# Performance work log

Measured on AMD Instinct MI355X. Metric: run time of the kernel, lower is better.

The kernel has to match this reference:

```python
import jax, jax.numpy as jnp
import numpy as np

EMBED = 64
HEADS = 8
DHEAD = EMBED // HEADS  # 8
LAYERS = 4
VOCAB = 32000
SEQ = 1024
BATCH = 8
EPS = 1e-5


def setup_inputs() -> dict:
    key = jax.random.key(0)
    ks = jax.random.split(key, 24)
    s = 0.02
    inp = {
        "x": jax.random.randint(ks[0], (BATCH, SEQ), 0, VOCAB),
        "targets": jax.random.randint(ks[1], (BATCH, SEQ), 0, VOCAB),
        "tok_emb": jax.random.normal(ks[2], (VOCAB, EMBED)) * s,
        "pos_emb": jax.random.normal(ks[3], (SEQ, EMBED)) * s,
        # per-layer, per-head q/k/v projections (stored as (in,out) so y = x @ W + b)
        "Wq": jax.random.normal(ks[4], (LAYERS, HEADS, EMBED, DHEAD)) * s,
        "bq": jax.random.normal(ks[5], (LAYERS, HEADS, DHEAD)) * s,
        "Wk": jax.random.normal(ks[6], (LAYERS, HEADS, EMBED, DHEAD)) * s,
        "bk": jax.random.normal(ks[7], (LAYERS, HEADS, DHEAD)) * s,
        "Wv": jax.random.normal(ks[8], (LAYERS, HEADS, EMBED, DHEAD)) * s,
        "bv": jax.random.normal(ks[9], (LAYERS, HEADS, DHEAD)) * s,
        "ln1_g": jnp.ones((LAYERS, EMBED)) + jax.random.normal(ks[10], (LAYERS, EMBED)) * s,
        "ln1_b": jax.random.normal(ks[11], (LAYERS, EMBED)) * s,
        "ln2_g": jnp.ones((LAYERS, EMBED)) + jax.random.normal(ks[12], (LAYERS, EMBED)) * s,
        "ln2_b": jax.random.normal(ks[13], (LAYERS, EMBED)) * s,
        "W1": jax.random.normal(ks[14], (LAYERS, EMBED, 4 * EMBED)) * s,
        "b1": jax.random.normal(ks[15], (LAYERS, 4 * EMBED)) * s,
        "W2": jax.random.normal(ks[16], (LAYERS, 4 * EMBED, EMBED)) * s,
        "b2": jax.random.normal(ks[17], (LAYERS, EMBED)) * s,
        "Wout": jax.random.normal(ks[18], (EMBED, VOCAB)) * s,
        "bout": jax.random.normal(ks[19], (VOCAB,)) * s,
    }
    return inp


def _layernorm(x, g, b):
    mu = jnp.mean(x, axis=-1, keepdims=True)
    var = jnp.var(x, axis=-1, keepdims=True)
    return (x - mu) / jnp.sqrt(var + EPS) * g + b


def _mha(h, Wq, bq, Wk, bk, Wv, bv):
    B, T, C = h.shape
    q = jnp.einsum('btc,hcd->bhtd', h, Wq) + bq[:, None, :]
    k = jnp.einsum('btc,hcd->bhtd', h, Wk) + bk[:, None, :]
    v = jnp.einsum('btc,hcd->bhtd', h, Wv) + bv[:, None, :]
    # FAITHFUL to source: key output is .view(B, C, T) -- a raw reshape, not transpose
    kr = k.reshape(B, HEADS, DHEAD, T)
    w = jnp.einsum('bhtd,bhds->bhts', q, kr)  # [B,H,T,T]
    w = jnp.tril(w)
    w = jnp.where(w == 0, -jnp.inf, w)
    w = jax.nn.softmax(w / np.sqrt(DHEAD), axis=-1)
    o = jnp.einsum('bhts,bhsd->bhtd', w, v)
    return o.transpose(0, 2, 1, 3).reshape(B, T, HEADS * DHEAD)


def _forward(x, targets, tok_emb, pos_emb, Wq, bq, Wk, bk, Wv, bv,
             ln1_g, ln1_b, ln2_g, ln2_b, W1, b1, W2, b2, Wout, bout):
    B, T = x.shape
    h = tok_emb[x] + pos_emb[:T]
    for l in range(LAYERS):
        h = h + _layernorm(_mha(h, Wq[l], bq[l], Wk[l], bk[l], Wv[l], bv[l]), ln1_g[l], ln1_b[l])
        z = _layernorm(h, ln2_g[l], ln2_b[l])
        h = h + jax.nn.relu(z @ W1[l] + b1[l]) @ W2[l] + b2[l]
    logits = h @ Wout + bout  # [B,T,V]
    lp = jax.nn.log_softmax(logits.reshape(B * T, -1), axis=-1)
    nll = -jnp.take_along_axis(lp, targets.reshape(B * T, 1), axis=1)
    loss = jnp.mean(nll)
    return logits, loss


def reference(x, targets, tok_emb, pos_emb, Wq, bq, Wk, bk, Wv, bv,
              ln1_g, ln1_b, ln2_g, ln2_b, W1, b1, W2, b2, Wout, bout):
    return _forward(x, targets, tok_emb, pos_emb, Wq, bq, Wk, bk, Wv, bv,
                    ln1_g, ln1_b, ln2_g, ln2_b, W1, b1, W2, b2, Wout, bout)
```

## Files before the change

### kernel.cpp

```cpp
#include <hip/hip_runtime.h>
#include <hip/hip_bf16.h>
#include <math.h>

#define BB 8
#define TT 1024
#define CC 64
#define HH 8
#define DH 8
#define NLAY 4
#define VV 32000
#define FF 256
#define NR (BB*TT)
#define NLOGIT 262144000
#define NCB 125

typedef unsigned short u16;
typedef unsigned int u32;
typedef __attribute__((ext_vector_type(8))) short short8v;
typedef __attribute__((ext_vector_type(4))) float f32x4;

__device__ __forceinline__ float b2f(u16 u){
  union { float f; u32 i; } c; c.i = ((u32)u) << 16; return c.f;
}
__device__ __forceinline__ u16 f2b(float f){
  union { float f; u32 i; } c; c.f = f;
  u32 x = c.i;
  return (u16)((x + 0x7FFF + ((x >> 16) & 1)) >> 16);
}
__device__ __forceinline__ u32 pack2(float lo, float hi){
  return (u32)f2b(lo) | ((u32)f2b(hi) << 16);
}

__global__ void k_probe(const void* ln1g, int* flag){
  if (threadIdx.x == 0 && blockIdx.x == 0){
    const u16* p = (const u16*)ln1g;
    int cnt = 0;
    for (int i = 0; i < 256; i++){ if ((p[i] >> 8) == 0x3F) cnt++; }
    *flag = (cnt > 192) ? 1 : 0;
  }
}

struct ConvArgs {
  const void* src[18];
  float* dst[18];
  int n[18];
  int blkoff[19];
  const int* flag;
  u16* wt16;
};
__global__ void k_convert(ConvArgs a){
  int isb = *a.flag;
  int bid = blockIdx.x;
  int t = 0;
  while (bid >= a.blkoff[t + 1]) t++;
  int base = (bid - a.blkoff[t]) * 1024 + threadIdx.x;
  const u16* s16 = (const u16*)a.src[t];
  const float* s32 = (const float*)a.src[t];
  float* d = a.dst[t];
  int n = a.n[t];
  #pragma unroll
  for (int e = 0; e < 4; e++){
    int i = base + e * 256;
    if (i < n){
      float v = isb ? b2f(s16[i]) : s32[i];
      d[i] = v;
      if (t == 16){
        int k = i / VV, col = i - k * VV;
        a.wt16[(size_t)col * 64 + k] = f2b(v);
      }
    }
  }
}

__global__ void k_embed(const int* __restrict__ x, const float* __restrict__ tok,
                        const float* __restrict__ pos, float* __restrict__ h){
  int i = blockIdx.x * 256 + threadIdx.x;
  int r = i >> 6, c = i & 63;
  int t = r & (TT - 1);
  h[i] = tok[x[r] * 64 + c] + pos[t * 64 + c];
}

__global__ void k_qkv(const float* __restrict__ h,
                      const float* __restrict__ wq, const float* __restrict__ bq,
                      const float* __restrict__ wk, const float* __restrict__ bk,
                      const float* __restrict__ wv, const float* __restrict__ bv,
                      u16* __restrict__ q16, u16* __restrict__ kp16, u16* __restrict__ vt16){
  __shared__ float hs[4][64];
  int tid = threadIdx.x;
  int row0 = blockIdx.x * 4;
  hs[tid >> 6][tid & 63] = h[row0 * 64 + tid];
  __syncthreads();
  int rr = tid >> 6, o = tid & 63;
  int head = o >> 3, d = o & 7;
  int row = row0 + rr;
  int b = row >> 10, t = row & (TT - 1);
  float aq = bq[head * 8 + d], ak = bk[head * 8 + d], av = bv[head * 8 + d];
  #pragma unroll
  for (int c = 0; c < 64; c++){
    float hv = hs[rr][c];
    aq += hv * wq[(head * 64 + c) * 8 + d];
    ak += hv * wk[(head * 64 + c) * 8 + d];
    av += hv * wv[(head * 64 + c) * 8 + d];
  }
  int bh = b * HH + head;
  q16[((size_t)bh * TT + t) * 8 + d] = f2b(aq * 0.35355339059327378f);
  int i = t * 8 + d;
  kp16[((size_t)bh * TT + (i & 1023)) * 8 + (i >> 10)] = f2b(ak);
  vt16[((size_t)bh * 8 + d) * TT + t] = f2b(av);
}

__global__ void __launch_bounds__(64) k_attn(const u16* __restrict__ q16, const u16* __restrict__ kp16,
                                             const u16* __restrict__ vt16, float* __restrict__ att){
  int lane = threadIdx.x & 63;
  int lr = lane & 15, lg = lane >> 4;
  int bh = blockIdx.y;
  int tb = blockIdx.x * 16;
  int t_g = tb + lr;

  short8v qf = {0,0,0,0,0,0,0,0};
  if (lg == 0) qf = *(const short8v*)(q16 + ((size_t)bh * TT + tb + lr) * 8);

  float m = -1e30f, l = 0.f;
  f32x4 o = {0.f, 0.f, 0.f, 0.f};
  int nchunk = (tb >> 5) + 1;

  for (int c = 0; c < nchunk; c++){
    int s0 = c * 32;
    bool skipB = (s0 + 16 > tb + 15);
    short8v kA = {0,0,0,0,0,0,0,0}, kB = {0,0,0,0,0,0,0,0};
    if (lg == 0){
      kA = *(const short8v*)(kp16 + ((size_t)bh * TT + s0 + lr) * 8);
      if (!skipB) kB = *(const short8v*)(kp16 + ((size_t)bh * TT + s0 + 16 + lr) * 8);
    }
    f32x4 sA = __builtin_amdgcn_mfma_f32_16x16x32_bf16(kA, qf, (f32x4){0.f,0.f,0.f,0.f}, 0, 0, 0);
    f32x4 sB;
    if (!skipB)
      sB = __builtin_amdgcn_mfma_f32_16x16x32_bf16(kB, qf, (f32x4){0.f,0.f,0.f,0.f}, 0, 0, 0);
    else
      sB = (f32x4){-1e30f, -1e30f, -1e30f, -1e30f};

    if (s0 + 15 > tb){
      #pragma unroll
      for (int r = 0; r < 4; r++) if (s0 + lg * 4 + r > t_g) sA[r] = -1e30f;
    }
    if (!skipB && s0 + 31 > tb){
      #pragma unroll
      for (int r = 0; r < 4; r++) if (s0 + 16 + lg * 4 + r > t_g) sB[r] = -1e30f;
    }

    float tm = fmaxf(fmaxf(fmaxf(sA[0], sA[1]), fmaxf(sA[2], sA[3])),
                     fmaxf(fmaxf(sB[0], sB[1]), fmaxf(sB[2], sB[3])));
    tm = fmaxf(tm, __shfl_xor(tm, 16, 64));
    tm = fmaxf(tm, __shfl_xor(tm, 32, 64));
    float mn = fmaxf(m, tm);
    float fac = __expf(m - mn);
    l *= fac;
    {
      float f0 = __shfl(fac, lg * 4 + 0, 64);
      float f1 = __shfl(fac, lg * 4 + 1, 64);
      float f2 = __shfl(fac, lg * 4 + 2, 64);
      float f3 = __shfl(fac, lg * 4 + 3, 64);
      o[0] *= f0; o[1] *= f1; o[2] *= f2; o[3] *= f3;
    }
    f32x4 pA, pB;
    #pragma unroll
    for (int r = 0; r < 4; r++){ pA[r] = __expf(sA[r] - mn); pB[r] = __expf(sB[r] - mn); }
    float ls = pA[0] + pA[1] + pA[2] + pA[3] + pB[0] + pB[1] + pB[2] + pB[3];
    ls += __shfl_xor(ls, 16, 64);
    ls += __shfl_xor(ls, 32, 64);
    l += ls;
    m = mn;

    u32 a0 = pack2(pA[0], pA[1]), a1 = pack2(pA[2], pA[3]);
    u32 b0 = pack2(pB[0], pB[1]), b1 = pack2(pB[2], pB[3]);
    int src0 = ((2 * lg) & 3) * 16 + lr;
    int src1 = src0 + 16;
    u32 A0 = __shfl((int)a0, src0, 64), A1 = __shfl((int)a1, src0, 64);
    u32 A2 = __shfl((int)a0, src1, 64), A3 = __shfl((int)a1, src1, 64);
    u32 B0 = __shfl((int)b0, src0, 64), B1 = __shfl((int)b1, src0, 64);
    u32 B2 = __shfl((int)b0, src1, 64), B3 = __shfl((int)b1, src1, 64);
    union { u32 u[4]; short8v v; } pu;
    if (lg < 2){ pu.u[0] = A0; pu.u[1] = A1; pu.u[2] = A2; pu.u[3] = A3; }
    else       { pu.u[0] = B0; pu.u[1] = B1; pu.u[2] = B2; pu.u[3] = B3; }

    short8v vf = {0,0,0,0,0,0,0,0};
    if (lr < 8) vf = *(const short8v*)(vt16 + ((size_t)bh * 8 + lr) * TT + s0 + lg * 8);

    o = __builtin_amdgcn_mfma_f32_16x16x32_bf16(pu.v, vf, o, 0, 0, 0);
  }

  float linv = 1.f / l;
  float i0 = __shfl(linv, lg * 4 + 0, 64);
  float i1 = __shfl(linv, lg * 4 + 1, 64);
  float i2 = __shfl(linv, lg * 4 + 2, 64);
  float i3 = __shfl(linv, lg * 4 + 3, 64);
  if (lr < 8){
    int b = bh >> 3, head = bh & 7;
    float* op = att + ((size_t)b * TT + tb) * 64 + head * 8 + lr;
    op[(lg * 4 + 0) * 64] = o[0] * i0;
    op[(lg * 4 + 1) * 64] = o[1] * i1;
    op[(lg * 4 + 2) * 64] = o[2] * i2;
    op[(lg * 4 + 3) * 64] = o[3] * i3;
  }
}

__global__ void k_lnres(const float* __restrict__ src, const float* __restrict__ g,
                        const float* __restrict__ bb, float* __restrict__ h){
  int tid = threadIdx.x;
  int row = blockIdx.x * 4 + (tid >> 6);
  int lane = tid & 63;
  float x = src[row * 64 + lane];
  float s = x, sq = x * x;
  for (int msk = 32; msk; msk >>= 1){
    s += __shfl_xor(s, msk, 64);
    sq += __shfl_xor(sq, msk, 64);
  }
  float mu = s * (1.f / 64);
  float var = sq * (1.f / 64) - mu * mu;
  float rstd = rsqrtf(fmaxf(var, 0.f) + 1e-5f);
  h[row * 64 + lane] += (x - mu) * rstd * g[lane] + bb[lane];
}

__global__ void k_ffn(float* __restrict__ h, const float* __restrict__ g, const float* __restrict__ bb,
                      const float* __restrict__ w1, const float* __restrict__ b1,
                      const float* __restrict__ w2, const float* __restrict__ b2){
  __shared__ float z[8][64];
  __shared__ float a[8][256];
  int tid = threadIdx.x;
  int row0 = blockIdx.x * 8;
  {
    int rr = tid >> 5, cp = tid & 31;
    int c0 = cp * 2;
    const float* hp = h + (row0 + rr) * 64;
    float x0 = hp[c0], x1 = hp[c0 + 1];
    float s = x0 + x1, sq = x0 * x0 + x1 * x1;
    for (int msk = 16; msk; msk >>= 1){
      s += __shfl_xor(s, msk, 64);
      sq += __shfl_xor(sq, msk, 64);
    }
    float mu = s * (1.f / 64);
    float var = sq * (1.f / 64) - mu * mu;
    float rstd = rsqrtf(fmaxf(var, 0.f) + 1e-5f);
    z[rr][c0]     = (x0 - mu) * rstd * g[c0] + bb[c0];
    z[rr][c0 + 1] = (x1 - mu) * rstd * g[c0 + 1] + bb[c0 + 1];
  }
  __syncthreads();
  {
    int j = tid;
    float acc[8];
    float bj = b1[j];
    #pragma unroll
    for (int r = 0; r < 8; r++) acc[r] = bj;
    for (int c = 0; c < 64; c++){
      float w = w1[c * 256 + j];
      #pragma unroll
      for (int r = 0; r < 8; r++) acc[r] += z[r][c] * w;
    }
    #pragma unroll
    for (int r = 0; r < 8; r++) a[r][j] = fmaxf(acc[r], 0.f);
  }
  __syncthreads();
  #pragma unroll
  for (int half = 0; half < 2; half++){
    int oi = tid + half * 256;
    int r = oi >> 6, c = oi & 63;
    float acc = b2[c];
    for (int k = 0; k < 256; k++) acc += a[r][k] * w2[k * 64 + c];
    h[(row0 + r) * 64 + c] += acc;
  }
}

__global__ void k_h2b(const float* __restrict__ h, u16* __restrict__ hb){
  int i = blockIdx.x * 256 + threadIdx.x;
  hb[i] = f2b(h[i]);
}

__global__ void __launch_bounds__(256) k_logits(const u16* __restrict__ hb, const u16* __restrict__ wt,
                                                const float* __restrict__ bout, float* __restrict__ logits,
                                                float2* __restrict__ part){
  int tid = threadIdx.x;
  int wave = tid >> 6, lane = tid & 63;
  int lr = lane & 15, lg = lane >> 4;
  int row0 = blockIdx.y * 64;
  int colw = blockIdx.x * 256 + wave * 64;

  short8v af[4][2];
  #pragma unroll
  for (int mi = 0; mi < 4; mi++)
    #pragma unroll
    for (int kk = 0; kk < 2; kk++)
      af[mi][kk] = *(const short8v*)(hb + (row0 + mi * 16 + lr) * 64 + kk * 32 + lg * 8);

  short8v bf[4][2];
  #pragma unroll
  for (int nf = 0; nf < 4; nf++){
    int col = colw + nf * 16 + lr;
    #pragma unroll
    for (int kk = 0; kk < 2; kk++)
      bf[nf][kk] = *(const short8v*)(wt + (size_t)col * 64 + kk * 32 + lg * 8);
  }

  f32x4 acc[4][4];
  #pragma unroll
  for (int mi = 0; mi < 4; mi++)
    #pragma unroll
    for (int nf = 0; nf < 4; nf++)
      acc[mi][nf] = (f32x4){0.f, 0.f, 0.f, 0.f};

  #pragma unroll
  for (int mi = 0; mi < 4; mi++){
    #pragma unroll
    for (int nf = 0; nf < 4; nf++){
      acc[mi][nf] = __builtin_amdgcn_mfma_f32_16x16x32_bf16(af[mi][0], bf[nf][0], acc[mi][nf], 0, 0, 0);
      acc[mi][nf] = __builtin_amdgcn_mfma_f32_16x16x32_bf16(af[mi][1], bf[nf][1], acc[mi][nf], 0, 0, 0);
    }
  }

  float bo[4];
  #pragma unroll
  for (int nf = 0; nf < 4; nf++) bo[nf] = bout[colw + nf * 16 + lr];

  #pragma unroll
  for (int mi = 0; mi < 4; mi++){
    #pragma unroll
    for (int nf = 0; nf < 4; nf++){
      int colg = colw + nf * 16 + lr;
      #pragma unroll
      for (int r = 0; r < 4; r++){
        int rowg = row0 + mi * 16 + lg * 4 + r;
        logits[(size_t)rowg * VV + colg] = acc[mi][nf][r] + bo[nf];
      }
    }
  }

  __shared__ float2 wml[4][64];
  #pragma unroll
  for (int mi = 0; mi < 4; mi++){
    #pragma unroll
    for (int r = 0; r < 4; r++){
      float v0 = acc[mi][0][r] + bo[0], v1 = acc[mi][1][r] + bo[1];
      float v2 = acc[mi][2][r] + bo[2], v3 = acc[mi][3][r] + bo[3];
      float mx = fmaxf(fmaxf(v0, v1), fmaxf(v2, v3));
      for (int msk = 1; msk < 16; msk <<= 1) mx = fmaxf(mx, __shfl_xor(mx, msk, 64));
      float sume = __expf(v0 - mx) + __expf(v1 - mx) + __expf(v2 - mx) + __expf(v3 - mx);
      for (int msk = 1; msk < 16; msk <<= 1) sume += __shfl_xor(sume, msk, 64);
      if (lr == 0) wml[wave][mi * 16 + lg * 4 + r] = make_float2(mx, sume);
    }
  }
  __syncthreads();
  if (tid < 64){
    float M = -1e30f;
    #pragma unroll
    for (int w = 0; w < 4; w++) M = fmaxf(M, wml[w][tid].x);
    float L = 0.f;
    #pragma unroll
    for (int w = 0; w < 4; w++){
      float2 p = wml[w][tid];
      L += p.y * __expf(p.x - M);
    }
    part[(size_t)blockIdx.x * NR + row0 + tid] = make_float2(M, L);
  }
}

__global__ void k_loss(const float2* __restrict__ part, const float* __restrict__ logits,
                       const int* __restrict__ tgt, float* __restrict__ lpart){
  int row = blockIdx.x * 256 + threadIdx.x;
  float M = -1e30f;
  for (int j = 0; j < NCB; j++) M = fmaxf(M, part[(size_t)j * NR + row].x);
  float L = 0.f;
  for (int j = 0; j < NCB; j++){
    float2 p = part[(size_t)j * NR + row];
    L += p.y * __expf(p.x - M);
  }
  float lse = M + __logf(L);
  float tl = logits[(size_t)row * VV + tgt[row]];
  float nll = lse - tl;
  __shared__ float red[4];
  for (int msk = 32; msk; msk >>= 1) nll += __shfl_xor(nll, msk, 64);
  if ((threadIdx.x & 63) == 0) red[threadIdx.x >> 6] = nll;
  __syncthreads();
  if (threadIdx.x == 0) lpart[blockIdx.x] = red[0] + red[1] + red[2] + red[3];
}
__global__ void k_loss2(const float* __restrict__ lpart, float* __restrict__ out){
  if (threadIdx.x == 0 && blockIdx.x == 0){
    float s = 0.f;
    for (int i = 0; i < 32; i++) s += lpart[i];
    out[NLOGIT] = s * (1.f / NR);
  }
}

extern "C" void kernel_launch(void* const* d_in, const int* in_sizes, int n_in,
                              void* d_out, int out_size, void* d_ws, size_t ws_size,
                              hipStream_t stream){
  (void)in_sizes; (void)n_in; (void)out_size; (void)ws_size;
  const int* x = (const int*)d_in[0];
  const int* targets = (const int*)d_in[1];
  float* out = (float*)d_out;

  static const int WN[18] = {2048000, 65536, 16384, 256, 16384, 256, 16384, 256,
                             256, 256, 256, 256, 65536, 1024, 65536, 256, 2048000, 32000};
  char* ws = (char*)d_ws;
  size_t off = 0;
  auto alloc = [&](size_t bytes) -> void* {
    void* p = ws + off;
    off += (bytes + 255) & ~(size_t)255;
    return p;
  };
  int* flag = (int*)alloc(256);
  float* wf[18];
  for (int i = 0; i < 18; i++) wf[i] = (float*)alloc((size_t)WN[i] * 4);
  float* h     = (float*)alloc((size_t)NR * 64 * 4);
  float* att_o = (float*)alloc((size_t)NR * 64 * 4);
  u16* q16     = (u16*)alloc((size_t)NR * 64 * 2);
  u16* kp16    = (u16*)alloc((size_t)NR * 64 * 2);
  u16* vt16    = (u16*)alloc((size_t)NR * 64 * 2);
  u16* hb      = (u16*)alloc((size_t)NR * 64 * 2);
  u16* wt16    = (u16*)alloc((size_t)2048000 * 2);
  float2* part = (float2*)alloc((size_t)NCB * NR * 8);
  float* lpart = (float*)alloc(32 * 4);

  hipLaunchKernelGGL(k_probe, dim3(1), dim3(64), 0, stream, d_in[10], flag);
  ConvArgs ca;
  int blk = 0;
  for (int i = 0; i < 18; i++){
    ca.src[i] = d_in[2 + i];
    ca.dst[i] = wf[i];
    ca.n[i] = WN[i];
    ca.blkoff[i] = blk;
    blk += (WN[i] + 1023) / 1024;
  }
  ca.blkoff[18] = blk;
  ca.flag = flag;
  ca.wt16 = wt16;
  hipLaunchKernelGGL(k_convert, dim3(blk), dim3(256), 0, stream, ca);

  hipLaunchKernelGGL(k_embed, dim3(2048), dim3(256), 0, stream, x, wf[0], wf[1], h);

  for (int l = 0; l < NLAY; l++){
    hipLaunchKernelGGL(k_qkv, dim3(2048), dim3(256), 0, stream, h,
                       wf[2] + l * 4096, wf[3] + l * 64,
                       wf[4] + l * 4096, wf[5] + l * 64,
                       wf[6] + l * 4096, wf[7] + l * 64,
                       q16, kp16, vt16);
    hipLaunchKernelGGL(k_attn, dim3(64, 64), dim3(64), 0, stream, q16, kp16, vt16, att_o);
    hipLaunchKernelGGL(k_lnres, dim3(2048), dim3(256), 0, stream, att_o,
                       wf[8] + l * 64, wf[9] + l * 64, h);
    hipLaunchKernelGGL(k_ffn, dim3(1024), dim3(256), 0, stream, h,
                       wf[10] + l * 64, wf[11] + l * 64,
                       wf[12] + l * 16384, wf[13] + l * 256,
                       wf[14] + l * 16384, wf[15] + l * 64);
  }

  hipLaunchKernelGGL(k_h2b, dim3(2048), dim3(256), 0, stream, h, hb);
  hipLaunchKernelGGL(k_logits, dim3(NCB, 128), dim3(256), 0, stream, hb, wt16, wf[17], out, part);
  hipLaunchKernelGGL(k_loss, dim3(32), dim3(256), 0, stream, part, out, targets, lpart);
  hipLaunchKernelGGL(k_loss2, dim3(1), dim3(64), 0, stream, lpart, out);
}
```

Before: 792.0 us.

## Fuse attention with layernorm-residual, transpose Wout via LDS, restructure logits stores

Several independent changes land together. The probe kernel is folded into a per-block ballot. The scattered Wout transpose inside the convert kernel becomes a separate LDS-tiled transpose kernel. Attention now runs all 8 heads of a batch in one 512-thread block and applies the LN+residual in place, which drops the att_o buffer and the k_lnres launch. The final FFN layer writes the bf16 hidden state directly instead of running k_h2b. The logits MFMA operands are swapped so each lane holds 4 contiguous columns, allowing vectorized nontemporal stores with a new grid order, and the loss reduction launches are reshaped. These changes add code complexity and raise register and LDS pressure in the fused attention block.

Result: faster. 735.2 us (-7.2%).

```diff
diff --git a/kernel.cpp b/kernel.cpp
--- a/kernel.cpp
+++ b/kernel.cpp
@@ -30,14 +30,10 @@
 __device__ __forceinline__ u32 pack2(float lo, float hi){
   return (u32)f2b(lo) | ((u32)f2b(hi) << 16);
 }
-
-__global__ void k_probe(const void* ln1g, int* flag){
-  if (threadIdx.x == 0 && blockIdx.x == 0){
-    const u16* p = (const u16*)ln1g;
-    int cnt = 0;
-    for (int i = 0; i < 256; i++){ if ((p[i] >> 8) == 0x3F) cnt++; }
-    *flag = (cnt > 192) ? 1 : 0;
-  }
+__device__ __forceinline__ int probe_bf16(const void* ln1g){
+  const u16* lp = (const u16*)ln1g;
+  unsigned long long m = __ballot((lp[threadIdx.x & 63] >> 8) == 0x3F);
+  return (__popcll(m) > 48) ? 1 : 0;
 }
 
 struct ConvArgs {
@@ -45,11 +41,9 @@
   float* dst[18];
   int n[18];
   int blkoff[19];
-  const int* flag;
-  u16* wt16;
 };
-__global__ void k_convert(ConvArgs a){
-  int isb = *a.flag;
+__global__ void k_convert(ConvArgs a, const void* ln1g){
+  int isb = probe_bf16(ln1g);
   int bid = blockIdx.x;
   int t = 0;
   while (bid >= a.blkoff[t + 1]) t++;
@@ -61,14 +55,31 @@
   #pragma unroll
   for (int e = 0; e < 4; e++){
     int i = base + e * 256;
-    if (i < n){
-      float v = isb ? b2f(s16[i]) : s32[i];
-      d[i] = v;
-      if (t == 16){
-        int k = i / VV, col = i - k * VV;
-        a.wt16[(size_t)col * 64 + k] = f2b(v);
-      }
-    }
+    if (i < n) d[i] = isb ? b2f(s16[i]) : s32[i];
+  }
+}
+
+__global__ void __launch_bounds__(256) k_trans(const void* __restrict__ wsrc, const void* __restrict__ ln1g,
+                                               u16* __restrict__ wt){
+  __shared__ float ws_[64][65];
+  int tid = threadIdx.x;
+  int isb = probe_bf16(ln1g);
+  int v0 = blockIdx.x * 64;
+  const u16* s16 = (const u16*)wsrc;
+  const float* s32 = (const float*)wsrc;
+  int vl = tid & 63;
+  #pragma unroll
+  for (int kk = 0; kk < 16; kk++){
+    int k = kk * 4 + (tid >> 6);
+    size_t idx = (size_t)k * VV + v0 + vl;
+    ws_[vl][k] = isb ? b2f(s16[idx]) : s32[idx];
+  }
+  __syncthreads();
+  #pragma unroll
+  for (int pass = 0; pass < 16; pass++){
+    int v2 = pass * 4 + (tid >> 6);
+    int k = tid & 63;
+    wt[(size_t)(v0 + v2) * 64 + k] = f2b(ws_[v2][k]);
   }
 }
 
@@ -109,11 +120,16 @@
   vt16[((size_t)bh * 8 + d) * TT + t] = f2b(av);
 }
 
-__global__ void __launch_bounds__(64) k_attn(const u16* __restrict__ q16, const u16* __restrict__ kp16,
-                                             const u16* __restrict__ vt16, float* __restrict__ att){
-  int lane = threadIdx.x & 63;
+__global__ void __launch_bounds__(512) k_attn2(const u16* __restrict__ q16, const u16* __restrict__ kp16,
+                                               const u16* __restrict__ vt16, const float* __restrict__ g,
+                                               const float* __restrict__ be, float* __restrict__ h){
+  __shared__ float ot[16][64];
+  int tid = threadIdx.x;
+  int w = tid >> 6;
+  int lane = tid & 63;
   int lr = lane & 15, lg = lane >> 4;
-  int bh = blockIdx.y;
+  int b = blockIdx.y;
+  int bh = b * HH + w;
   int tb = blockIdx.x * 16;
   int t_g = tb + lr;
 
@@ -195,35 +211,33 @@
   float i2 = __shfl(linv, lg * 4 + 2, 64);
   float i3 = __shfl(linv, lg * 4 + 3, 64);
   if (lr < 8){
-    int b = bh >> 3, head = bh & 7;
-    float* op = att + ((size_t)b * TT + tb) * 64 + head * 8 + lr;
-    op[(lg * 4 + 0) * 64] = o[0] * i0;
-    op[(lg * 4 + 1) * 64] = o[1] * i1;
-    op[(lg * 4 + 2) * 64] = o[2] * i2;
-    op[(lg * 4 + 3) * 64] = o[3] * i3;
-  }
-}
-
-__global__ void k_lnres(const float* __restrict__ src, const float* __restrict__ g,
-                        const float* __restrict__ bb, float* __restrict__ h){
-  int tid = threadIdx.x;
-  int row = blockIdx.x * 4 + (tid >> 6);
-  int lane = tid & 63;
-  float x = src[row * 64 + lane];
-  float s = x, sq = x * x;
-  for (int msk = 32; msk; msk >>= 1){
-    s += __shfl_xor(s, msk, 64);
-    sq += __shfl_xor(sq, msk, 64);
-  }
-  float mu = s * (1.f / 64);
-  float var = sq * (1.f / 64) - mu * mu;
-  float rstd = rsqrtf(fmaxf(var, 0.f) + 1e-5f);
-  h[row * 64 + lane] += (x - mu) * rstd * g[lane] + bb[lane];
+    ot[lg * 4 + 0][w * 8 + lr] = o[0] * i0;
+    ot[lg * 4 + 1][w * 8 + lr] = o[1] * i1;
+    ot[lg * 4 + 2][w * 8 + lr] = o[2] * i2;
+    ot[lg * 4 + 3][w * 8 + lr] = o[3] * i3;
+  }
+  __syncthreads();
+
+  #pragma unroll
+  for (int pass = 0; pass < 2; pass++){
+    int rl = (tid >> 6) + pass * 8;
+    float x = ot[rl][lane];
+    float s = x, sq = x * x;
+    for (int msk = 32; msk; msk >>= 1){
+      s += __shfl_xor(s, msk, 64);
+      sq += __shfl_xor(sq, msk, 64);
+    }
+    float mu = s * (1.f / 64);
+    float var = sq * (1.f / 64) - mu * mu;
+    float rstd = rsqrtf(fmaxf(var, 0.f) + 1e-5f);
+    h[((size_t)b * TT + tb + rl) * 64 + lane] += (x - mu) * rstd * g[lane] + be[lane];
+  }
 }
 
 __global__ void k_ffn(float* __restrict__ h, const float* __restrict__ g, const float* __restrict__ bb,
                       const float* __restrict__ w1, const float* __restrict__ b1,
-                      const float* __restrict__ w2, const float* __restrict__ b2){
+                      const float* __restrict__ w2, const float* __restrict__ b2,
+                      u16* __restrict__ hbo, int last){
   __shared__ float z[8][64];
   __shared__ float a[8][256];
   int tid = threadIdx.x;
@@ -266,13 +280,11 @@
     int r = oi >> 6, c = oi & 63;
     float acc = b2[c];
     for (int k = 0; k < 256; k++) acc += a[r][k] * w2[k * 64 + c];
-    h[(row0 + r) * 64 + c] += acc;
-  }
-}
-
-__global__ void k_h2b(const float* __restrict__ h, u16* __restrict__ hb){
-  int i = blockIdx.x * 256 + threadIdx.x;
-  hb[i] = f2b(h[i]);
+    int gi = (row0 + r) * 64 + c;
+    float nh = h[gi] + acc;
+    h[gi] = nh;
+    if (last) hbo[gi] = f2b(nh);
+  }
 }
 
 __global__ void __launch_bounds__(256) k_logits(const u16* __restrict__ hb, const u16* __restrict__ wt,
@@ -281,71 +293,70 @@
   int tid = threadIdx.x;
   int wave = tid >> 6, lane = tid & 63;
   int lr = lane & 15, lg = lane >> 4;
-  int row0 = blockIdx.y * 64;
-  int colw = blockIdx.x * 256 + wave * 64;
-
-  short8v af[4][2];
-  #pragma unroll
-  for (int mi = 0; mi < 4; mi++)
+  int row0 = blockIdx.x * 64;
+  int cb = blockIdx.y;
+  int colw = cb * 256 + wave * 64;
+
+  short8v hf[4][2];
+  #pragma unroll
+  for (int ri = 0; ri < 4; ri++)
     #pragma unroll
     for (int kk = 0; kk < 2; kk++)
-      af[mi][kk] = *(const short8v*)(hb + (row0 + mi * 16 + lr) * 64 + kk * 32 + lg * 8);
-
-  short8v bf[4][2];
-  #pragma unroll
-  for (int nf = 0; nf < 4; nf++){
-    int col = colw + nf * 16 + lr;
+      hf[ri][kk] = *(const short8v*)(hb + (row0 + ri * 16 + lr) * 64 + kk * 32 + lg * 8);
+
+  short8v wfr[4][2];
+  #pragma unroll
+  for (int vi = 0; vi < 4; vi++)
     #pragma unroll
     for (int kk = 0; kk < 2; kk++)
-      bf[nf][kk] = *(const short8v*)(wt + (size_t)col * 64 + kk * 32 + lg * 8);
-  }
+      wfr[vi][kk] = *(const short8v*)(wt + (size_t)(colw + vi * 16 + lr) * 64 + kk * 32 + lg * 8);
 
   f32x4 acc[4][4];
   #pragma unroll
-  for (int mi = 0; mi < 4; mi++)
-    #pragma unroll
-    for (int nf = 0; nf < 4; nf++)
-      acc[mi][nf] = (f32x4){0.f, 0.f, 0.f, 0.f};
-
-  #pragma unroll
-  for (int mi = 0; mi < 4; mi++){
-    #pragma unroll
-    for (int nf = 0; nf < 4; nf++){
-      acc[mi][nf] = __builtin_amdgcn_mfma_f32_16x16x32_bf16(af[mi][0], bf[nf][0], acc[mi][nf], 0, 0, 0);
-      acc[mi][nf] = __builtin_amdgcn_mfma_f32_16x16x32_bf16(af[mi][1], bf[nf][1], acc[mi][nf], 0, 0, 0);
-    }
-  }
-
-  float bo[4];
-  #pragma unroll
-  for (int nf = 0; nf < 4; nf++) bo[nf] = bout[colw + nf * 16 + lr];
-
-  #pragma unroll
-  for (int mi = 0; mi < 4; mi++){
-    #pragma unroll
-    for (int nf = 0; nf < 4; nf++){
-      int colg = colw + nf * 16 + lr;
+  for (int ri = 0; ri < 4; ri++)
+    #pragma unroll
+    for (int vi = 0; vi < 4; vi++)
+      acc[ri][vi] = (f32x4){0.f, 0.f, 0.f, 0.f};
+
+  #pragma unroll
+  for (int ri = 0; ri < 4; ri++){
+    #pragma unroll
+    for (int vi = 0; vi < 4; vi++){
+      acc[ri][vi] = __builtin_amdgcn_mfma_f32_16x16x32_bf16(wfr[vi][0], hf[ri][0], acc[ri][vi], 0, 0, 0);
+      acc[ri][vi] = __builtin_amdgcn_mfma_f32_16x16x32_bf16(wfr[vi][1], hf[ri][1], acc[ri][vi], 0, 0, 0);
+    }
+  }
+
+  f32x4 bo[4];
+  #pragma unroll
+  for (int vi = 0; vi < 4; vi++)
+    bo[vi] = *(const f32x4*)(bout + colw + vi * 16 + lg * 4);
+
+  __shared__ float2 wml[4][64];
+  #pragma unroll
+  for (int ri = 0; ri < 4; ri++){
+    f32x4 vals[4];
+    #pragma unroll
+    for (int vi = 0; vi < 4; vi++){
+      vals[vi] = acc[ri][vi] + bo[vi];
+      __builtin_nontemporal_store(vals[vi],
+        (f32x4*)(logits + (size_t)(row0 + ri * 16 + lr) * VV + colw + vi * 16 + lg * 4));
+    }
+    float mx = -1e30f;
+    #pragma unroll
+    for (int vi = 0; vi < 4; vi++)
       #pragma unroll
-      for (int r = 0; r < 4; r++){
-        int rowg = row0 + mi * 16 + lg * 4 + r;
-        logits[(size_t)rowg * VV + colg] = acc[mi][nf][r] + bo[nf];
-      }
-    }
-  }
-
-  __shared__ float2 wml[4][64];
-  #pragma unroll
-  for (int mi = 0; mi < 4; mi++){
-    #pragma unroll
-    for (int r = 0; r < 4; r++){
-      float v0 = acc[mi][0][r] + bo[0], v1 = acc[mi][1][r] + bo[1];
-      float v2 = acc[mi][2][r] + bo[2], v3 = acc[mi][3][r] + bo[3];
-      float mx = fmaxf(fmaxf(v0, v1), fmaxf(v2, v3));
-      for (int msk = 1; msk < 16; msk <<= 1) mx = fmaxf(mx, __shfl_xor(mx, msk, 64));
-      float sume = __expf(v0 - mx) + __expf(v1 - mx) + __expf(v2 - mx) + __expf(v3 - mx);
-      for (int msk = 1; msk < 16; msk <<= 1) sume += __shfl_xor(sume, msk, 64);
-      if (lr == 0) wml[wave][mi * 16 + lg * 4 + r] = make_float2(mx, sume);
-    }
+      for (int r = 0; r < 4; r++) mx = fmaxf(mx, vals[vi][r]);
+    mx = fmaxf(mx, __shfl_xor(mx, 16, 64));
+    mx = fmaxf(mx, __shfl_xor(mx, 32, 64));
+    float sume = 0.f;
+    #pragma unroll
+    for (int vi = 0; vi < 4; vi++)
+      #pragma unroll
+      for (int r = 0; r < 4; r++) sume += __expf(vals[vi][r] - mx);
+    sume += __shfl_xor(sume, 16, 64);
+    sume += __shfl_xor(sume, 32, 64);
+    if (lg == 0) wml[wave][ri * 16 + lr] = make_float2(mx, sume);
   }
   __syncthreads();
   if (tid < 64){
@@ -358,13 +369,13 @@
       float2 p = wml[w][tid];
       L += p.y * __expf(p.x - M);
     }
-    part[(size_t)blockIdx.x * NR + row0 + tid] = make_float2(M, L);
+    part[(size_t)cb * NR + row0 + tid] = make_float2(M, L);
   }
 }
 
 __global__ void k_loss(const float2* __restrict__ part, const float* __restrict__ logits,
                        const int* __restrict__ tgt, float* __restrict__ lpart){
-  int row = blockIdx.x * 256 + threadIdx.x;
+  int row = blockIdx.x * 64 + (threadIdx.x & 63);
   float M = -1e30f;
   for (int j = 0; j < NCB; j++) M = fmaxf(M, part[(size_t)j * NR + row].x);
   float L = 0.f;
@@ -375,18 +386,14 @@
   float lse = M + __logf(L);
   float tl = logits[(size_t)row * VV + tgt[row]];
   float nll = lse - tl;
-  __shared__ float red[4];
   for (int msk = 32; msk; msk >>= 1) nll += __shfl_xor(nll, msk, 64);
-  if ((threadIdx.x & 63) == 0) red[threadIdx.x >> 6] = nll;
-  __syncthreads();
-  if (threadIdx.x == 0) lpart[blockIdx.x] = red[0] + red[1] + red[2] + red[3];
+  if ((threadIdx.x & 63) == 0) lpart[blockIdx.x] = nll;
 }
 __global__ void k_loss2(const float* __restrict__ lpart, float* __restrict__ out){
-  if (threadIdx.x == 0 && blockIdx.x == 0){
-    float s = 0.f;
-    for (int i = 0; i < 32; i++) s += lpart[i];
-    out[NLOGIT] = s * (1.f / NR);
-  }
+  int lane = threadIdx.x & 63;
+  float s = lpart[lane] + lpart[lane + 64];
+  for (int msk = 32; msk; msk >>= 1) s += __shfl_xor(s, msk, 64);
+  if (lane == 0) out[NLOGIT] = s * (1.f / NR);
 }
 
 extern "C" void kernel_launch(void* const* d_in, const int* in_sizes, int n_in,
@@ -398,7 +405,7 @@
   float* out = (float*)d_out;
 
   static const int WN[18] = {2048000, 65536, 16384, 256, 16384, 256, 16384, 256,
-                             256, 256, 256, 256, 65536, 1024, 65536, 256, 2048000, 32000};
+                             256, 256, 256, 256, 65536, 1024, 65536, 256, 0, 32000};
   char* ws = (char*)d_ws;
   size_t off = 0;
   auto alloc = [&](size_t bytes) -> void* {
@@ -406,20 +413,17 @@
     off += (bytes + 255) & ~(size_t)255;
     return p;
   };
-  int* flag = (int*)alloc(256);
   float* wf[18];
-  for (int i = 0; i < 18; i++) wf[i] = (float*)alloc((size_t)WN[i] * 4);
+  for (int i = 0; i < 18; i++) wf[i] = (float*)alloc((size_t)(WN[i] ? WN[i] : 1) * 4);
   float* h     = (float*)alloc((size_t)NR * 64 * 4);
-  float* att_o = (float*)alloc((size_t)NR * 64 * 4);
   u16* q16     = (u16*)alloc((size_t)NR * 64 * 2);
   u16* kp16    = (u16*)alloc((size_t)NR * 64 * 2);
   u16* vt16    = (u16*)alloc((size_t)NR * 64 * 2);
   u16* hb      = (u16*)alloc((size_t)NR * 64 * 2);
   u16* wt16    = (u16*)alloc((size_t)2048000 * 2);
   float2* part = (float2*)alloc((size_t)NCB * NR * 8);
-  float* lpart = (float*)alloc(32 * 4);
-
-  hipLaunchKernelGGL(k_probe, dim3(1), dim3(64), 0, stream, d_in[10], flag);
+  float* lpart = (float*)alloc(128 * 4);
+
   ConvArgs ca;
   int blk = 0;
   for (int i = 0; i < 18; i++){
@@ -430,10 +434,8 @@
     blk += (WN[i] + 1023) / 1024;
   }
   ca.blkoff[18] = blk;
-  ca.flag = flag;
-  ca.wt16 = wt16;
-  hipLaunchKernelGGL(k_convert, dim3(blk), dim3(256), 0, stream, ca);
-
+  hipLaunchKernelGGL(k_convert, dim3(blk), dim3(256), 0, stream, ca, d_in[10]);
+  hipLaunchKernelGGL(k_trans, dim3(500), dim3(256), 0, stream, d_in[18], d_in[10], wt16);
   hipLaunchKernelGGL(k_embed, dim3(2048), dim3(256), 0, stream, x, wf[0], wf[1], h);
 
   for (int l = 0; l < NLAY; l++){
@@ -442,17 +444,16 @@
                        wf[4] + l * 4096, wf[5] + l * 64,
                        wf[6] + l * 4096, wf[7] + l * 64,
                        q16, kp16, vt16);
-    hipLaunchKernelGGL(k_attn, dim3(64, 64), dim3(64), 0, stream, q16, kp16, vt16, att_o);
-    hipLaunchKernelGGL(k_lnres, dim3(2048), dim3(256), 0, stream, att_o,
+    hipLaunchKernelGGL(k_attn2, dim3(64, 8), dim3(512), 0, stream, q16, kp16, vt16,
                        wf[8] + l * 64, wf[9] + l * 64, h);
     hipLaunchKernelGGL(k_ffn, dim3(1024), dim3(256), 0, stream, h,
                        wf[10] + l * 64, wf[11] + l * 64,
                        wf[12] + l * 16384, wf[13] + l * 256,
-                       wf[14] + l * 16384, wf[15] + l * 64);
-  }
-
-  hipLaunchKernelGGL(k_h2b, dim3(2048), dim3(256), 0, stream, h, hb);
-  hipLaunchKernelGGL(k_logits, dim3(NCB, 128), dim3(256), 0, stream, hb, wt16, wf[17], out, part);
-  hipLaunchKernelGGL(k_loss, dim3(32), dim3(256), 0, stream, part, out, targets, lpart);
+                       wf[14] + l * 16384, wf[15] + l * 64,
+                       hb, (l == NLAY - 1) ? 1 : 0);
+  }
+
+  hipLaunchKernelGGL(k_logits, dim3(128, NCB), dim3(256), 0, stream, hb, wt16, wf[17], out, part);
+  hipLaunchKernelGGL(k_loss, dim3(128), dim3(64), 0, stream, part, out, targets, lpart);
   hipLaunchKernelGGL(k_loss2, dim3(1), dim3(64), 0, stream, lpart, out);
 }
```
